# Optimization experiments

Hardware: AMD Instinct MI355X
Metric: run time of the kernel (lower is better)

## Reference

```python
import jax, jax.numpy as jnp
import numpy as np
from jax import lax

WINDOW_SIZE = 11
SIGMA = 1.5
RGB_RANGE = 1.0
K1, K2 = 0.01, 0.03
CHANNELS = 3


def gaussian_window(window_size, sigma, channels, dtype=jnp.float32):
    coords = jnp.arange(window_size, dtype=dtype) - window_size // 2
    g = jnp.exp(-(coords ** 2) / (2.0 * sigma * sigma))
    g = g / g.sum()
    w2d = jnp.outer(g, g)
    w2d = w2d / w2d.sum()
    # depthwise kernel: (C, 1, ws, ws) in OIHW with feature_group_count=C
    return jnp.broadcast_to(w2d, (channels, 1, window_size, window_size)).astype(dtype)


def _dwconv(inp, window, padding):
    # depthwise conv2d, groups = C
    C = inp.shape[1]
    return lax.conv_general_dilated(
        inp, window,
        window_strides=(1, 1),
        padding=[(padding, padding), (padding, padding)],
        feature_group_count=C,
        dimension_numbers=('NCHW', 'OIHW', 'NCHW'))


def setup_inputs() -> dict:
    key = jax.random.key(0)
    kx, ky = jax.random.split(key)
    B, C, H, W = 16, CHANNELS, 512, 512
    x = jax.random.uniform(kx, (B, C, H, W), dtype=jnp.float32)
    y = jax.random.uniform(ky, (B, C, H, W), dtype=jnp.float32)
    window = gaussian_window(WINDOW_SIZE, SIGMA, C)
    return {"x": x, "y": y, "window": window}


def reference(x, y, window):
    padding = WINDOW_SIZE // 2
    mu_x = _dwconv(x, window, padding)
    mu_y = _dwconv(y, window, padding)
    mu_x2 = mu_x * mu_x
    mu_y2 = mu_y * mu_y
    mu_xy = mu_x * mu_y
    sigma_x2 = _dwconv(x * x, window, padding) - mu_x2
    sigma_y2 = _dwconv(y * y, window, padding) - mu_y2
    sigma_xy = _dwconv(x * y, window, padding) - mu_xy
    L = RGB_RANGE
    C1 = (K1 * L) ** 2
    C2 = (K2 * L) ** 2
    ssim_map = ((2.0 * mu_xy + C1) * (2.0 * sigma_xy + C2)) / (
        (mu_x2 + mu_y2 + C1) * (sigma_x2 + sigma_y2 + C2) + 1e-12)
    loss = 1.0 - ssim_map
    return loss.mean()
```

## Files before the change

kernel.cpp:

```cpp
#include <hip/hip_runtime.h>


typedef _Float16 h2 __attribute__((ext_vector_type(2)));
typedef __fp16 fp16x2 __attribute__((ext_vector_type(2)));

__device__ __forceinline__ unsigned h2u(h2 v) { return __builtin_bit_cast(unsigned, v); }
__device__ __forceinline__ unsigned h2u(fp16x2 v) { return __builtin_bit_cast(unsigned, v); }
__device__ __forceinline__ h2 u2h(unsigned u) { return __builtin_bit_cast(h2, u); }

__device__ __forceinline__ float fdot2_(h2 a, h2 b, float c) {
#if defined(__has_builtin) && __has_builtin(__builtin_amdgcn_fdot2)
    return __builtin_amdgcn_fdot2(a, b, c, false);
#else
    return fmaf((float)a[1], (float)b[1], fmaf((float)a[0], (float)b[0], c));
#endif
}

#define SXW 26
#define HPW 36

__global__ __launch_bounds__(256, 4) void ssim_main(
    const float* __restrict__ xg, const float* __restrict__ yg,
    const float* __restrict__ w2d, float* __restrict__ part)
{
    __shared__ __align__(16) uint2 sxy2[42 * SXW];
    __shared__ __align__(16) unsigned hp[5 * 21 * HPW];
    __shared__ float gs[11];
    __shared__ float wred[4];

    const int tid = threadIdx.x;

    if (tid < 11) {
        float s = 0.0f;
        #pragma unroll
        for (int j = 0; j < 11; ++j) s += w2d[tid * 11 + j];
        gs[tid] = s;
    }

    const int x0 = blockIdx.x * 32 - 5;
    const int y0 = blockIdx.y * 32 - 5;
    const size_t zoff = (size_t)blockIdx.z * (512 * 512);
    const float* __restrict__ xp = xg + zoff;
    const float* __restrict__ yp = yg + zoff;

    for (int it = tid; it < 42 * 24; it += 256) {
        const int r = it / 24, t = it - r * 24;
        const int gr = y0 + r, gc = x0 + 2 * t;
        const bool rok = (unsigned)gr < 512u;
        const int o = gr * 512 + gc;
        float xv0 = 0.f, xv1 = 0.f, yv0 = 0.f, yv1 = 0.f;
        if (rok && (unsigned)gc < 512u)       { xv0 = xp[o];     yv0 = yp[o]; }
        if (rok && (unsigned)(gc + 1) < 512u) { xv1 = xp[o + 1]; yv1 = yp[o + 1]; }
        sxy2[r * SXW + t] = make_uint2(
            h2u(__builtin_amdgcn_cvt_pkrtz(xv0, xv1)),
            h2u(__builtin_amdgcn_cvt_pkrtz(yv0, yv1)));
    }
    __syncthreads();

    h2 ge[6], go[6];
    {
        float gf[11]; float ssum = 0.0f;
        #pragma unroll
        for (int k = 0; k < 11; ++k) {
            gf[k] = (float)(_Float16)gs[k];
            if (k != 5) ssum += gf[k];
        }
        gf[5] = 1.0f - ssum;
        _Float16 gh[12];
        #pragma unroll
        for (int k = 0; k < 11; ++k) gh[k] = (_Float16)gf[k];
        gh[11] = (_Float16)0.0f;
        #pragma unroll
        for (int t = 0; t < 6; ++t) {
            ge[t][0] = gh[2 * t]; ge[t][1] = gh[2 * t + 1];
            go[t][0] = (t == 0) ? (_Float16)0.0f : gh[2 * t - 1];
            go[t][1] = (t == 0) ? gh[0] : gh[2 * t];
        }
    }

    auto conv4 = [&](const h2* s, float* o4) {
        float e0 = 0.f, o1 = 0.f, e2 = 0.f, o3 = 0.f;
        #pragma unroll
        for (int t = 0; t < 6; ++t) {
            e0 = fdot2_(ge[t], s[t],     e0);
            o1 = fdot2_(go[t], s[t],     o1);
            e2 = fdot2_(ge[t], s[t + 1], e2);
            o3 = fdot2_(go[t], s[t + 1], o3);
        }
        o4[0] = e0; o4[1] = o1; o4[2] = e2; o4[3] = o3;
    };

    if (tid < 21 * 8) {
        const int rp = tid >> 3, cq = tid & 7;
        float hv[2][5][4];
        #pragma unroll
        for (int e = 0; e < 2; ++e) {
            const int r = 2 * rp + e;
            const uint4* P = (const uint4*)&sxy2[r * SXW + 2 * cq];
            const uint4 A0 = P[0], A1 = P[1], A2 = P[2], A3 = P[3];
            h2 xh[8], yh[8];
            xh[0] = u2h(A0.x); yh[0] = u2h(A0.y); xh[1] = u2h(A0.z); yh[1] = u2h(A0.w);
            xh[2] = u2h(A1.x); yh[2] = u2h(A1.y); xh[3] = u2h(A1.z); yh[3] = u2h(A1.w);
            xh[4] = u2h(A2.x); yh[4] = u2h(A2.y); xh[5] = u2h(A2.z); yh[5] = u2h(A2.w);
            xh[6] = u2h(A3.x); yh[6] = u2h(A3.y); xh[7] = u2h(A3.z); yh[7] = u2h(A3.w);
            h2 xx[7], yy[7], xy[7];
            #pragma unroll
            for (int t = 0; t < 7; ++t) {
                xx[t] = xh[t] * xh[t];
                yy[t] = yh[t] * yh[t];
                xy[t] = xh[t] * yh[t];
            }
            conv4(xh, hv[e][0]);
            conv4(yh, hv[e][1]);
            conv4(xx, hv[e][2]);
            conv4(yy, hv[e][3]);
            conv4(xy, hv[e][4]);
        }
        #pragma unroll
        for (int qq = 0; qq < 5; ++qq) {
            uint4 w;
            w.x = h2u(__builtin_amdgcn_cvt_pkrtz(hv[0][qq][0], hv[1][qq][0]));
            w.y = h2u(__builtin_amdgcn_cvt_pkrtz(hv[0][qq][1], hv[1][qq][1]));
            w.z = h2u(__builtin_amdgcn_cvt_pkrtz(hv[0][qq][2], hv[1][qq][2]));
            w.w = h2u(__builtin_amdgcn_cvt_pkrtz(hv[0][qq][3], hv[1][qq][3]));
            *(uint4*)&hp[(qq * 21 + rp) * HPW + 4 * cq] = w;
        }
    }
    __syncthreads();

    const int r = tid >> 3, cq = tid & 7, m = r >> 1;
    h2 gsel[6];
    #pragma unroll
    for (int t = 0; t < 6; ++t) gsel[t] = (r & 1) ? go[t] : ge[t];

    float acc[5][4];
    #pragma unroll
    for (int qq = 0; qq < 5; ++qq) {
        float a0 = 0.f, a1 = 0.f, a2 = 0.f, a3 = 0.f;
        #pragma unroll
        for (int t = 0; t < 6; ++t) {
            const uint4 V = *(const uint4*)&hp[(qq * 21 + m + t) * HPW + 4 * cq];
            a0 = fdot2_(gsel[t], u2h(V.x), a0);
            a1 = fdot2_(gsel[t], u2h(V.y), a1);
            a2 = fdot2_(gsel[t], u2h(V.z), a2);
            a3 = fdot2_(gsel[t], u2h(V.w), a3);
        }
        acc[qq][0] = a0; acc[qq][1] = a1; acc[qq][2] = a2; acc[qq][3] = a3;
    }

    float lsum = 0.0f;
    const float C1 = 1e-4f, C2 = 9e-4f;
    #pragma unroll
    for (int j = 0; j < 4; ++j) {
        const float mx = acc[0][j], my = acc[1][j];
        const float exx = acc[2][j], eyy = acc[3][j], exy = acc[4][j];
        const float mx2 = mx * mx, my2 = my * my, mxy = mx * my;
        const float vx = exx - mx2, vy = eyy - my2, vxy = exy - mxy;
        const float num = (2.0f * mxy + C1) * (2.0f * vxy + C2);
        const float den = (mx2 + my2 + C1) * (vx + vy + C2) + 1e-12f;
        lsum = fmaf(num, __builtin_amdgcn_rcpf(den), lsum);
    }

    #pragma unroll
    for (int off = 32; off > 0; off >>= 1)
        lsum += __shfl_down(lsum, off, 64);
    if ((tid & 63) == 0) wred[tid >> 6] = lsum;
    __syncthreads();
    if (tid == 0) {
        const int bid = (blockIdx.z * gridDim.y + blockIdx.y) * gridDim.x
                        + blockIdx.x;
        part[bid] = wred[0] + wred[1] + wred[2] + wred[3];
    }
}

__global__ __launch_bounds__(256) void ssim_reduce(
    const float* __restrict__ part, float* __restrict__ out,
    int n, float invN)
{
    __shared__ float wred[4];
    float s = 0.0f;
    for (int i = threadIdx.x; i < n; i += 256) s += part[i];
    #pragma unroll
    for (int off = 32; off > 0; off >>= 1)
        s += __shfl_down(s, off, 64);
    if ((threadIdx.x & 63) == 0) wred[threadIdx.x >> 6] = s;
    __syncthreads();
    if (threadIdx.x == 0)
        out[0] = 1.0f - (wred[0] + wred[1] + wred[2] + wred[3]) * invN;
}

extern "C" void kernel_launch(void* const* d_in, const int* in_sizes, int n_in,
                              void* d_out, int out_size, void* d_ws, size_t ws_size,
                              hipStream_t stream) {
    const float* x   = (const float*)d_in[0];
    const float* y   = (const float*)d_in[1];
    const float* w2d = (const float*)d_in[2];
    float* out  = (float*)d_out;
    float* part = (float*)d_ws;

    const int H = 512, W = 512;
    const int total = in_sizes[0];
    const int Z = total / (H * W);

    dim3 grid(W / 32, H / 32, Z);
    const int nblocks = (W / 32) * (H / 32) * Z;
    ssim_main<<<grid, 256, 0, stream>>>(x, y, w2d, part);

    const float invN = 1.0f / (float)total;
    ssim_reduce<<<1, 256, 0, stream>>>(part, out, nblocks, invN);
}
```

Before: 174.6 us.

## Switch separable SSIM conv to packed fp16 FMA with wider 64x32 tiles

Replaces the fdot2-based horizontal and vertical passes with packed half-precision FMAs that accumulate in fp16, using pixel-pair packing and shifted pairs for the odd taps. Tiles widen to 64 columns to cut halo overhead, and a branch-free load path is added for interior tiles. The vertical pass is done by 128 threads, each producing 4 rows by 4 columns. Accumulating in fp16 lowers precision for variance terms computed as E[x^2]-mu^2, and leaving half the threads idle in the final pass may reduce parallelism.

```diff
diff --git a/kernel.cpp b/kernel.cpp
--- a/kernel.cpp
+++ b/kernel.cpp
@@ -2,30 +2,30 @@
 
 
 typedef _Float16 h2 __attribute__((ext_vector_type(2)));
-typedef __fp16 fp16x2 __attribute__((ext_vector_type(2)));
 
 __device__ __forceinline__ unsigned h2u(h2 v) { return __builtin_bit_cast(unsigned, v); }
-__device__ __forceinline__ unsigned h2u(fp16x2 v) { return __builtin_bit_cast(unsigned, v); }
 __device__ __forceinline__ h2 u2h(unsigned u) { return __builtin_bit_cast(h2, u); }
-
-__device__ __forceinline__ float fdot2_(h2 a, h2 b, float c) {
-#if defined(__has_builtin) && __has_builtin(__builtin_amdgcn_fdot2)
-    return __builtin_amdgcn_fdot2(a, b, c, false);
-#else
-    return fmaf((float)a[1], (float)b[1], fmaf((float)a[0], (float)b[0], c));
-#endif
-}
-
-#define SXW 26
-#define HPW 36
-
-__global__ __launch_bounds__(256, 4) void ssim_main(
+__device__ __forceinline__ unsigned shp(unsigned lo, unsigned hi) {
+    return (lo >> 16) | (hi << 16);
+}
+__device__ __forceinline__ h2 pkfma(h2 a, h2 b, h2 c) {
+    return __builtin_elementwise_fma(a, b, c);
+}
+__device__ __forceinline__ unsigned pk2(float a, float b) {
+    return h2u((h2){(_Float16)a, (_Float16)b});
+}
+
+#define SXP 40
+#define HPS 36
+
+__global__ __launch_bounds__(256) void ssim_main(
     const float* __restrict__ xg, const float* __restrict__ yg,
     const float* __restrict__ w2d, float* __restrict__ part)
 {
-    __shared__ __align__(16) uint2 sxy2[42 * SXW];
-    __shared__ __align__(16) unsigned hp[5 * 21 * HPW];
-    __shared__ float gs[11];
+    __shared__ __align__(16) unsigned sxp[42 * SXP];
+    __shared__ __align__(16) unsigned syp[42 * SXP];
+    __shared__ __align__(16) unsigned hq[5][42 * HPS];
+    __shared__ float gsf[11];
     __shared__ float wred[4];
 
     const int tid = threadIdx.x;
@@ -34,131 +34,145 @@
         float s = 0.0f;
         #pragma unroll
         for (int j = 0; j < 11; ++j) s += w2d[tid * 11 + j];
-        gs[tid] = s;
-    }
-
-    const int x0 = blockIdx.x * 32 - 5;
+        gsf[tid] = s;
+    }
+
+    const int x0 = blockIdx.x * 64 - 5;
     const int y0 = blockIdx.y * 32 - 5;
     const size_t zoff = (size_t)blockIdx.z * (512 * 512);
     const float* __restrict__ xp = xg + zoff;
     const float* __restrict__ yp = yg + zoff;
 
-    for (int it = tid; it < 42 * 24; it += 256) {
-        const int r = it / 24, t = it - r * 24;
-        const int gr = y0 + r, gc = x0 + 2 * t;
-        const bool rok = (unsigned)gr < 512u;
-        const int o = gr * 512 + gc;
-        float xv0 = 0.f, xv1 = 0.f, yv0 = 0.f, yv1 = 0.f;
-        if (rok && (unsigned)gc < 512u)       { xv0 = xp[o];     yv0 = yp[o]; }
-        if (rok && (unsigned)(gc + 1) < 512u) { xv1 = xp[o + 1]; yv1 = yp[o + 1]; }
-        sxy2[r * SXW + t] = make_uint2(
-            h2u(__builtin_amdgcn_cvt_pkrtz(xv0, xv1)),
-            h2u(__builtin_amdgcn_cvt_pkrtz(yv0, yv1)));
-    }
-    __syncthreads();
-
-    h2 ge[6], go[6];
+    const bool interior = (x0 >= 0) & (x0 + 73 < 512) & (y0 >= 0) & (y0 + 41 < 512);
+    if (interior) {
+        for (int it = tid; it < 42 * 37; it += 256) {
+            const int r = it / 37, p = it - r * 37;
+            const int o = (y0 + r) * 512 + x0 + 2 * p;
+            sxp[r * SXP + p] = pk2(xp[o], xp[o + 1]);
+            syp[r * SXP + p] = pk2(yp[o], yp[o + 1]);
+        }
+    } else {
+        for (int it = tid; it < 42 * 37; it += 256) {
+            const int r = it / 37, p = it - r * 37;
+            const int gr = y0 + r, gc = x0 + 2 * p;
+            const bool rok = (unsigned)gr < 512u;
+            const int o = gr * 512 + gc;
+            float xv0 = 0.f, xv1 = 0.f, yv0 = 0.f, yv1 = 0.f;
+            if (rok && (unsigned)gc < 512u)       { xv0 = xp[o];     yv0 = yp[o]; }
+            if (rok && (unsigned)(gc + 1) < 512u) { xv1 = xp[o + 1]; yv1 = yp[o + 1]; }
+            sxp[r * SXP + p] = pk2(xv0, xv1);
+            syp[r * SXP + p] = pk2(yv0, yv1);
+        }
+    }
+    __syncthreads();
+
+    h2 g2[11];
     {
-        float gf[11]; float ssum = 0.0f;
+        _Float16 gh[11]; float ssum = 0.0f;
         #pragma unroll
         for (int k = 0; k < 11; ++k) {
-            gf[k] = (float)(_Float16)gs[k];
-            if (k != 5) ssum += gf[k];
-        }
-        gf[5] = 1.0f - ssum;
-        _Float16 gh[12];
-        #pragma unroll
-        for (int k = 0; k < 11; ++k) gh[k] = (_Float16)gf[k];
-        gh[11] = (_Float16)0.0f;
-        #pragma unroll
-        for (int t = 0; t < 6; ++t) {
-            ge[t][0] = gh[2 * t]; ge[t][1] = gh[2 * t + 1];
-            go[t][0] = (t == 0) ? (_Float16)0.0f : gh[2 * t - 1];
-            go[t][1] = (t == 0) ? gh[0] : gh[2 * t];
-        }
-    }
-
-    auto conv4 = [&](const h2* s, float* o4) {
-        float e0 = 0.f, o1 = 0.f, e2 = 0.f, o3 = 0.f;
-        #pragma unroll
-        for (int t = 0; t < 6; ++t) {
-            e0 = fdot2_(ge[t], s[t],     e0);
-            o1 = fdot2_(go[t], s[t],     o1);
-            e2 = fdot2_(ge[t], s[t + 1], e2);
-            o3 = fdot2_(go[t], s[t + 1], o3);
-        }
-        o4[0] = e0; o4[1] = o1; o4[2] = e2; o4[3] = o3;
-    };
-
-    if (tid < 21 * 8) {
-        const int rp = tid >> 3, cq = tid & 7;
-        float hv[2][5][4];
-        #pragma unroll
-        for (int e = 0; e < 2; ++e) {
-            const int r = 2 * rp + e;
-            const uint4* P = (const uint4*)&sxy2[r * SXW + 2 * cq];
-            const uint4 A0 = P[0], A1 = P[1], A2 = P[2], A3 = P[3];
-            h2 xh[8], yh[8];
-            xh[0] = u2h(A0.x); yh[0] = u2h(A0.y); xh[1] = u2h(A0.z); yh[1] = u2h(A0.w);
-            xh[2] = u2h(A1.x); yh[2] = u2h(A1.y); xh[3] = u2h(A1.z); yh[3] = u2h(A1.w);
-            xh[4] = u2h(A2.x); yh[4] = u2h(A2.y); xh[5] = u2h(A2.z); yh[5] = u2h(A2.w);
-            xh[6] = u2h(A3.x); yh[6] = u2h(A3.y); xh[7] = u2h(A3.z); yh[7] = u2h(A3.w);
-            h2 xx[7], yy[7], xy[7];
-            #pragma unroll
-            for (int t = 0; t < 7; ++t) {
-                xx[t] = xh[t] * xh[t];
-                yy[t] = yh[t] * yh[t];
-                xy[t] = xh[t] * yh[t];
-            }
-            conv4(xh, hv[e][0]);
-            conv4(yh, hv[e][1]);
-            conv4(xx, hv[e][2]);
-            conv4(yy, hv[e][3]);
-            conv4(xy, hv[e][4]);
-        }
-        #pragma unroll
-        for (int qq = 0; qq < 5; ++qq) {
-            uint4 w;
-            w.x = h2u(__builtin_amdgcn_cvt_pkrtz(hv[0][qq][0], hv[1][qq][0]));
-            w.y = h2u(__builtin_amdgcn_cvt_pkrtz(hv[0][qq][1], hv[1][qq][1]));
-            w.z = h2u(__builtin_amdgcn_cvt_pkrtz(hv[0][qq][2], hv[1][qq][2]));
-            w.w = h2u(__builtin_amdgcn_cvt_pkrtz(hv[0][qq][3], hv[1][qq][3]));
-            *(uint4*)&hp[(qq * 21 + rp) * HPW + 4 * cq] = w;
-        }
-    }
-    __syncthreads();
-
-    const int r = tid >> 3, cq = tid & 7, m = r >> 1;
-    h2 gsel[6];
-    #pragma unroll
-    for (int t = 0; t < 6; ++t) gsel[t] = (r & 1) ? go[t] : ge[t];
-
-    float acc[5][4];
-    #pragma unroll
-    for (int qq = 0; qq < 5; ++qq) {
-        float a0 = 0.f, a1 = 0.f, a2 = 0.f, a3 = 0.f;
-        #pragma unroll
-        for (int t = 0; t < 6; ++t) {
-            const uint4 V = *(const uint4*)&hp[(qq * 21 + m + t) * HPW + 4 * cq];
-            a0 = fdot2_(gsel[t], u2h(V.x), a0);
-            a1 = fdot2_(gsel[t], u2h(V.y), a1);
-            a2 = fdot2_(gsel[t], u2h(V.z), a2);
-            a3 = fdot2_(gsel[t], u2h(V.w), a3);
-        }
-        acc[qq][0] = a0; acc[qq][1] = a1; acc[qq][2] = a2; acc[qq][3] = a3;
-    }
+            gh[k] = (_Float16)gsf[k];
+            if (k != 5) ssum += (float)gh[k];
+        }
+        gh[5] = (_Float16)(1.0f - ssum);
+        #pragma unroll
+        for (int k = 0; k < 11; ++k) g2[k] = (h2){gh[k], gh[k]};
+    }
+
+    for (int it = tid; it < 42 * 8; it += 256) {
+        const int r = it >> 3, co = it & 7;
+        const int base = r * SXP + 4 * co;
+        unsigned X[12], Y[12];
+        *(uint4*)&X[0] = *(const uint4*)&sxp[base];
+        *(uint4*)&X[4] = *(const uint4*)&sxp[base + 4];
+        *(uint4*)&X[8] = *(const uint4*)&sxp[base + 8];
+        *(uint4*)&Y[0] = *(const uint4*)&syp[base];
+        *(uint4*)&Y[4] = *(const uint4*)&syp[base + 4];
+        *(uint4*)&Y[8] = *(const uint4*)&syp[base + 8];
+
+        const int ob = r * HPS + 4 * co;
+        auto run_q = [&](const unsigned* St, int qi) {
+            unsigned Sh[8];
+            #pragma unroll
+            for (int i = 0; i < 8; ++i) Sh[i] = shp(St[i], St[i + 1]);
+            h2 a[4];
+            #pragma unroll
+            for (int j = 0; j < 4; ++j) a[j] = (h2){(_Float16)0.f, (_Float16)0.f};
+            #pragma unroll
+            for (int k = 0; k < 11; ++k) {
+                #pragma unroll
+                for (int j = 0; j < 4; ++j) {
+                    const unsigned P = (k & 1) ? Sh[j + (k >> 1)] : St[j + (k >> 1)];
+                    a[j] = pkfma(g2[k], u2h(P), a[j]);
+                }
+            }
+            *(uint4*)&hq[qi][ob] = make_uint4(h2u(a[0]), h2u(a[1]), h2u(a[2]), h2u(a[3]));
+        };
+
+        run_q(X, 0);
+        run_q(Y, 1);
+        unsigned XX[9], YY[9], XY[9];
+        #pragma unroll
+        for (int i = 0; i < 9; ++i) {
+            const h2 xv = u2h(X[i]), yv = u2h(Y[i]);
+            XX[i] = h2u(xv * xv);
+            YY[i] = h2u(yv * yv);
+            XY[i] = h2u(xv * yv);
+        }
+        run_q(XX, 2);
+        run_q(YY, 3);
+        run_q(XY, 4);
+    }
+    __syncthreads();
 
     float lsum = 0.0f;
-    const float C1 = 1e-4f, C2 = 9e-4f;
-    #pragma unroll
-    for (int j = 0; j < 4; ++j) {
-        const float mx = acc[0][j], my = acc[1][j];
-        const float exx = acc[2][j], eyy = acc[3][j], exy = acc[4][j];
-        const float mx2 = mx * mx, my2 = my * my, mxy = mx * my;
-        const float vx = exx - mx2, vy = eyy - my2, vxy = exy - mxy;
-        const float num = (2.0f * mxy + C1) * (2.0f * vxy + C2);
-        const float den = (mx2 + my2 + C1) * (vx + vy + C2) + 1e-12f;
-        lsum = fmaf(num, __builtin_amdgcn_rcpf(den), lsum);
+    if (tid < 128) {
+        const int rq = tid >> 4, cqd = tid & 15;
+        h2 A[5][4][2];
+        #pragma unroll
+        for (int q = 0; q < 5; ++q)
+            #pragma unroll
+            for (int e = 0; e < 4; ++e) {
+                A[q][e][0] = (h2){(_Float16)0.f, (_Float16)0.f};
+                A[q][e][1] = (h2){(_Float16)0.f, (_Float16)0.f};
+            }
+        #pragma unroll
+        for (int j = 0; j < 14; ++j) {
+            const int ro = (4 * rq + j) * HPS + 2 * cqd;
+            #pragma unroll
+            for (int q = 0; q < 5; ++q) {
+                const uint2 V = *(const uint2*)&hq[q][ro];
+                const h2 p0 = u2h(V.x), p1 = u2h(V.y);
+                #pragma unroll
+                for (int e = 0; e < 4; ++e) {
+                    const int k = j - e;
+                    if (k >= 0 && k <= 10) {
+                        A[q][e][0] = pkfma(g2[k], p0, A[q][e][0]);
+                        A[q][e][1] = pkfma(g2[k], p1, A[q][e][1]);
+                    }
+                }
+            }
+        }
+        const float C1 = 1e-4f, C2 = 9e-4f;
+        #pragma unroll
+        for (int e = 0; e < 4; ++e) {
+            #pragma unroll
+            for (int pr = 0; pr < 2; ++pr) {
+                #pragma unroll
+                for (int el = 0; el < 2; ++el) {
+                    const float mx  = (float)A[0][e][pr][el];
+                    const float my  = (float)A[1][e][pr][el];
+                    const float exx = (float)A[2][e][pr][el];
+                    const float eyy = (float)A[3][e][pr][el];
+                    const float exy = (float)A[4][e][pr][el];
+                    const float mx2 = mx * mx, my2 = my * my, mxy = mx * my;
+                    const float vx = exx - mx2, vy = eyy - my2, vxy = exy - mxy;
+                    const float num = (2.0f * mxy + C1) * (2.0f * vxy + C2);
+                    const float den = (mx2 + my2 + C1) * (vx + vy + C2) + 1e-12f;
+                    lsum = fmaf(num, __builtin_amdgcn_rcpf(den), lsum);
+                }
+            }
+        }
     }
 
     #pragma unroll
@@ -202,8 +216,8 @@
     const int total = in_sizes[0];
     const int Z = total / (H * W);
 
-    dim3 grid(W / 32, H / 32, Z);
-    const int nblocks = (W / 32) * (H / 32) * Z;
+    dim3 grid(W / 64, H / 32, Z);
+    const int nblocks = (W / 64) * (H / 32) * Z;
     ssim_main<<<grid, 256, 0, stream>>>(x, y, w2d, part);
 
     const float invN = 1.0f / (float)total;
```

After: 192.6 us. +10.3%, slower.
